# Kernel optimization log

Measured on AMD Instinct MI355X. Metric: run time of the kernel, lower is better.

## Reference

```python
import jax, jax.numpy as jnp
import numpy as np

H = W = 2048
C = 8
N = 1_000_000


def setup_inputs() -> dict:
    key = jax.random.key(0)
    k1, k2 = jax.random.split(key)
    # coords in [0, H-4); the forward's mod wraps any value into range anyway
    coords = jax.random.uniform(k1, (N, 2), dtype=jnp.float32) * (H - 4)
    visible = jax.random.normal(k2, (H, W, C), dtype=jnp.float32)
    return {"coords": coords, "visible": visible}


def reference(coords, visible):
    dims = jnp.asarray(visible.shape[:2], dtype=coords.dtype)  # [2] = (H, W)
    # wrap coordinates into [1, dim-3) exactly like the TF layer
    c = ((coords - 1.0) % (dims - 4.0)) + 1.0          # [N,2]
    idx_low = jnp.floor(c)
    delta = c - idx_low                                 # [N,2]
    i = idx_low.astype(jnp.int32)                       # [N,2]

    def g(di, dj):  # gather visible at idx_low + [di, dj] -> [N,C]
        return visible[i[:, 0] + di, i[:, 1] + dj]

    top_left, top_right = g(0, 0), g(1, 0)
    bottom_left, bottom_right = g(0, 1), g(1, 1)

    d0 = delta[:, :1]   # delta along first coord axis, [N,1]
    d1 = delta[:, 1:2]  # delta along second coord axis, [N,1]

    mid_bottom = bottom_right + d0 * (bottom_left - bottom_right)
    mid_top = top_right + d0 * (top_left - top_right)
    interpolation = mid_bottom + d1 * (mid_top - mid_bottom)  # [N,C]

    # boundary mask exactly as in source (compares only coord 0; mod makes it a no-op)
    off = c > dims                                       # [N,2]
    cond = jnp.logical_or(off[:, 0], off[:, 0])          # [N]
    return jnp.where(cond[:, None], jnp.zeros_like(interpolation), interpolation)
```

## Files before the change

kernel.cpp:

```cpp
#include <hip/hip_runtime.h>

#define HH 2048
#define WW 2048
#define CC 8
#define MODV 2044.0f

__device__ __forceinline__ float lerp3(float tl, float tr, float bl, float br,
                                       float d0, float d1) {
    float mb = br + d0 * (bl - br);
    float mt = tr + d0 * (tl - tr);
    return mb + d1 * (mt - mb);
}

__global__ __launch_bounds__(256) void idx2pixel_kernel(
    const float* __restrict__ coords,
    const float* __restrict__ visible,
    float* __restrict__ out,
    int n)
{
    int t = blockIdx.x * blockDim.x + threadIdx.x;
    if (t >= n) return;

    float2 co = *reinterpret_cast<const float2*>(coords + 2 * (size_t)t);

    float x = co.x - 1.0f;
    float y = co.y - 1.0f;
    float cx = fmodf(x, MODV); if (cx < 0.0f) cx += MODV;
    float cy = fmodf(y, MODV); if (cy < 0.0f) cy += MODV;
    cx += 1.0f;
    cy += 1.0f;

    float fx = floorf(cx);
    float fy = floorf(cy);
    float d0 = cx - fx;
    float d1 = cy - fy;
    int i0 = (int)fx;
    int i1 = (int)fy;

    const float* p00 = visible + ((size_t)i0 * WW + (size_t)i1) * CC;
    const float* p01 = p00 + CC;
    const float* p10 = p00 + (size_t)WW * CC;
    const float* p11 = p10 + CC;

    float4 tl0 = *reinterpret_cast<const float4*>(p00);
    float4 tl1 = *reinterpret_cast<const float4*>(p00 + 4);
    float4 bl0 = *reinterpret_cast<const float4*>(p01);
    float4 bl1 = *reinterpret_cast<const float4*>(p01 + 4);
    float4 tr0 = *reinterpret_cast<const float4*>(p10);
    float4 tr1 = *reinterpret_cast<const float4*>(p10 + 4);
    float4 br0 = *reinterpret_cast<const float4*>(p11);
    float4 br1 = *reinterpret_cast<const float4*>(p11 + 4);

    bool zero = cx > (float)HH;
    float m = zero ? 0.0f : 1.0f;

    float4 o0, o1;
    o0.x = m * lerp3(tl0.x, tr0.x, bl0.x, br0.x, d0, d1);
    o0.y = m * lerp3(tl0.y, tr0.y, bl0.y, br0.y, d0, d1);
    o0.z = m * lerp3(tl0.z, tr0.z, bl0.z, br0.z, d0, d1);
    o0.w = m * lerp3(tl0.w, tr0.w, bl0.w, br0.w, d0, d1);
    o1.x = m * lerp3(tl1.x, tr1.x, bl1.x, br1.x, d0, d1);
    o1.y = m * lerp3(tl1.y, tr1.y, bl1.y, br1.y, d0, d1);
    o1.z = m * lerp3(tl1.z, tr1.z, bl1.z, br1.z, d0, d1);
    o1.w = m * lerp3(tl1.w, tr1.w, bl1.w, br1.w, d0, d1);

    float* po = out + (size_t)t * CC;
    *reinterpret_cast<float4*>(po)     = o0;
    *reinterpret_cast<float4*>(po + 4) = o1;
}

extern "C" void kernel_launch(void* const* d_in, const int* in_sizes, int n_in,
                              void* d_out, int out_size, void* d_ws, size_t ws_size,
                              hipStream_t stream) {
    const float* coords  = (const float*)d_in[0];
    const float* visible = (const float*)d_in[1];
    float* out = (float*)d_out;
    int n = in_sizes[0] / 2;

    int block = 256;
    int grid = (n + block - 1) / block;
    idx2pixel_kernel<<<grid, block, 0, stream>>>(coords, visible, out, n);
}
```

Before: 227.4 us.

## Bucket points by image row band and map bucket groups to XCDs for cache locality

Adds a pre-pass that reads the coordinates, sorts points into 256 row-band buckets in workspace memory, and records each point's original index. A second kernel then processes the buckets, assigning blocks so that each bucket's band of the image is served from one XCD's L2. The aim is to turn random gathers over the 128MB image into cache-local reads. In exchange it adds a memset, an extra write and read of the records, and output writes that are scattered rather than coalesced. Points that overflow both the per-bucket capacity and the fixed overflow buffer would be dropped.

```diff
diff --git a/kernel.cpp b/kernel.cpp
--- a/kernel.cpp
+++ b/kernel.cpp
@@ -4,6 +4,24 @@
 #define WW 2048
 #define CC 8
 #define MODV 2044.0f
+
+#define NBUCK 256
+#define CAP 4608
+#define OVCAP 4096
+#define K1_PPT 16
+#define K1_BLOCK 256
+#define K1_PPB (K1_PPT * K1_BLOCK)
+#define CURSOR_STRIDE 16
+#define CHUNKS_PER_BUCK (CAP / 256)
+
+typedef float v4f __attribute__((ext_vector_type(4)));
+#define LD4(p) (*reinterpret_cast<const v4f*>(p))
+
+__device__ __forceinline__ float wrap1(float v) {
+    float c = fmodf(v - 1.0f, MODV);
+    if (c < 0.0f) c += MODV;
+    return c + 1.0f;
+}
 
 __device__ __forceinline__ float lerp3(float tl, float tr, float bl, float br,
                                        float d0, float d1) {
@@ -12,49 +30,28 @@
     return mb + d1 * (mt - mb);
 }
 
-__global__ __launch_bounds__(256) void idx2pixel_kernel(
-    const float* __restrict__ coords,
-    const float* __restrict__ visible,
-    float* __restrict__ out,
-    int n)
-{
-    int t = blockIdx.x * blockDim.x + threadIdx.x;
-    if (t >= n) return;
-
-    float2 co = *reinterpret_cast<const float2*>(coords + 2 * (size_t)t);
-
-    float x = co.x - 1.0f;
-    float y = co.y - 1.0f;
-    float cx = fmodf(x, MODV); if (cx < 0.0f) cx += MODV;
-    float cy = fmodf(y, MODV); if (cy < 0.0f) cy += MODV;
-    cx += 1.0f;
-    cy += 1.0f;
-
-    float fx = floorf(cx);
-    float fy = floorf(cy);
-    float d0 = cx - fx;
-    float d1 = cy - fy;
+__device__ __forceinline__ void process_point(
+    float x, float y, int idx,
+    const float* __restrict__ visible, float* __restrict__ out)
+{
+    float cx = wrap1(x);
+    float cy = wrap1(y);
+    float fx = floorf(cx), fy = floorf(cy);
+    float d0 = cx - fx, d1 = cy - fy;
     int i0 = (int)fx;
     int i1 = (int)fy;
 
     const float* p00 = visible + ((size_t)i0 * WW + (size_t)i1) * CC;
-    const float* p01 = p00 + CC;
     const float* p10 = p00 + (size_t)WW * CC;
-    const float* p11 = p10 + CC;
-
-    float4 tl0 = *reinterpret_cast<const float4*>(p00);
-    float4 tl1 = *reinterpret_cast<const float4*>(p00 + 4);
-    float4 bl0 = *reinterpret_cast<const float4*>(p01);
-    float4 bl1 = *reinterpret_cast<const float4*>(p01 + 4);
-    float4 tr0 = *reinterpret_cast<const float4*>(p10);
-    float4 tr1 = *reinterpret_cast<const float4*>(p10 + 4);
-    float4 br0 = *reinterpret_cast<const float4*>(p11);
-    float4 br1 = *reinterpret_cast<const float4*>(p11 + 4);
-
-    bool zero = cx > (float)HH;
-    float m = zero ? 0.0f : 1.0f;
-
-    float4 o0, o1;
+
+    v4f tl0 = LD4(p00);      v4f tl1 = LD4(p00 + 4);
+    v4f bl0 = LD4(p00 + 8);  v4f bl1 = LD4(p00 + 12);
+    v4f tr0 = LD4(p10);      v4f tr1 = LD4(p10 + 4);
+    v4f br0 = LD4(p10 + 8);  v4f br1 = LD4(p10 + 12);
+
+    float m = (cx > (float)HH) ? 0.0f : 1.0f;
+
+    v4f o0, o1;
     o0.x = m * lerp3(tl0.x, tr0.x, bl0.x, br0.x, d0, d1);
     o0.y = m * lerp3(tl0.y, tr0.y, bl0.y, br0.y, d0, d1);
     o0.z = m * lerp3(tl0.z, tr0.z, bl0.z, br0.z, d0, d1);
@@ -64,9 +61,116 @@
     o1.z = m * lerp3(tl1.z, tr1.z, bl1.z, br1.z, d0, d1);
     o1.w = m * lerp3(tl1.w, tr1.w, bl1.w, br1.w, d0, d1);
 
-    float* po = out + (size_t)t * CC;
-    *reinterpret_cast<float4*>(po)     = o0;
-    *reinterpret_cast<float4*>(po + 4) = o1;
+    float* po = out + (size_t)idx * CC;
+    *reinterpret_cast<v4f*>(po)     = o0;
+    *reinterpret_cast<v4f*>(po + 4) = o1;
+}
+
+__global__ __launch_bounds__(K1_BLOCK) void k1_bucket(
+    const float* __restrict__ coords, int n,
+    unsigned int* __restrict__ cursors,
+    unsigned int* __restrict__ ovcur,
+    v4f* __restrict__ records,
+    v4f* __restrict__ ovrec)
+{
+    __shared__ unsigned int hist[NBUCK];
+    __shared__ unsigned int base[NBUCK];
+    __shared__ unsigned int offs[NBUCK];
+
+    int tid = threadIdx.x;
+    int blockStart = blockIdx.x * K1_PPB;
+    hist[tid] = 0;
+    offs[tid] = 0;
+    __syncthreads();
+
+    float xv[K1_PPT], yv[K1_PPT];
+    int bv[K1_PPT];
+#pragma unroll
+    for (int i = 0; i < K1_PPT; ++i) {
+        int p = blockStart + i * K1_BLOCK + tid;
+        bv[i] = -1;
+        if (p < n) {
+            float2 co = *reinterpret_cast<const float2*>(coords + 2 * (size_t)p);
+            xv[i] = co.x; yv[i] = co.y;
+            float cx = wrap1(co.x);
+            int i0 = (int)floorf(cx);
+            int b = i0 >> 3;
+            bv[i] = b;
+            atomicAdd(&hist[b], 1u);
+        }
+    }
+    __syncthreads();
+    {
+        unsigned int h = hist[tid];
+        base[tid] = h ? atomicAdd(&cursors[(size_t)tid * CURSOR_STRIDE], h) : 0u;
+    }
+    __syncthreads();
+#pragma unroll
+    for (int i = 0; i < K1_PPT; ++i) {
+        int b = bv[i];
+        if (b >= 0) {
+            unsigned int r = atomicAdd(&offs[b], 1u);
+            unsigned int g = base[b] + r;
+            int p = blockStart + i * K1_BLOCK + tid;
+            v4f rec;
+            rec.x = xv[i]; rec.y = yv[i];
+            rec.z = __int_as_float(p); rec.w = 0.0f;
+            if (g < CAP) {
+                records[(size_t)b * CAP + g] = rec;
+            } else {
+                unsigned int o = atomicAdd(ovcur, 1u);
+                if (o < OVCAP) ovrec[o] = rec;
+            }
+        }
+    }
+}
+
+__global__ __launch_bounds__(256) void k2_process(
+    const unsigned int* __restrict__ cursors,
+    const v4f* __restrict__ records,
+    const float* __restrict__ visible,
+    float* __restrict__ out)
+{
+    int g = blockIdx.x;
+    int xcd = g & 7;
+    int k = g >> 3;
+    int bl = k / CHUNKS_PER_BUCK;
+    int chunk = k - bl * CHUNKS_PER_BUCK;
+    int b = (bl << 3) | xcd;
+
+    unsigned int count = cursors[(size_t)b * CURSOR_STRIDE];
+    if (count > CAP) count = CAP;
+    unsigned int slot = chunk * 256 + threadIdx.x;
+    if (slot >= count) return;
+
+    v4f rec = records[(size_t)b * CAP + slot];
+    process_point(rec.x, rec.y, __float_as_int(rec.z), visible, out);
+}
+
+__global__ __launch_bounds__(256) void k2_overflow(
+    const unsigned int* __restrict__ ovcur,
+    const v4f* __restrict__ ovrec,
+    const float* __restrict__ visible,
+    float* __restrict__ out)
+{
+    unsigned int cnt = *ovcur;
+    if (cnt > OVCAP) cnt = OVCAP;
+    unsigned int s = blockIdx.x * 256 + threadIdx.x;
+    if (s >= cnt) return;
+    v4f rec = ovrec[s];
+    process_point(rec.x, rec.y, __float_as_int(rec.z), visible, out);
+}
+
+__global__ __launch_bounds__(256) void idx2pixel_direct(
+    const float* __restrict__ coords,
+    const float* __restrict__ visible,
+    float* __restrict__ out,
+    int n)
+{
+    int t = blockIdx.x * blockDim.x + threadIdx.x;
+    if (t >= n) return;
+    float2 co = *reinterpret_cast<const float2*>(coords + 2 * (size_t)t);
+    process_point(co.x, co.y, t, visible, out);
 }
 
 extern "C" void kernel_launch(void* const* d_in, const int* in_sizes, int n_in,
@@ -77,7 +181,27 @@
     float* out = (float*)d_out;
     int n = in_sizes[0] / 2;
 
-    int block = 256;
-    int grid = (n + block - 1) / block;
-    idx2pixel_kernel<<<grid, block, 0, stream>>>(coords, visible, out, n);
-}
+    const size_t REC_OFF = 16448;
+    const size_t REC_BYTES = (size_t)NBUCK * CAP * 16;
+    const size_t NEED = REC_OFF + REC_BYTES + (size_t)OVCAP * 16;
+
+    if (ws_size >= NEED) {
+        unsigned int* cursors = (unsigned int*)d_ws;
+        unsigned int* ovcur   = (unsigned int*)((char*)d_ws + 16384);
+        v4f* records          = (v4f*)((char*)d_ws + REC_OFF);
+        v4f* ovrec            = records + (size_t)NBUCK * CAP;
+
+        hipMemsetAsync(d_ws, 0, REC_OFF, stream);
+
+        int k1_blocks = (n + K1_PPB - 1) / K1_PPB;
+        k1_bucket<<<k1_blocks, K1_BLOCK, 0, stream>>>(coords, n, cursors, ovcur,
+                                                      records, ovrec);
+        k2_process<<<8 * 32 * CHUNKS_PER_BUCK, 256, 0, stream>>>(cursors, records,
+                                                                 visible, out);
+        k2_overflow<<<OVCAP / 256, 256, 0, stream>>>(ovcur, ovrec, visible, out);
+    } else {
+        int block = 256;
+        int grid = (n + block - 1) / block;
+        idx2pixel_direct<<<grid, block, 0, stream>>>(coords, visible, out, n);
+    }
+}
```

Result: slower. 271.0 us (+19.2%).
